# Kernel tuning notes

Hardware: AMD Instinct MI355X
Metric: run time of the kernel (lower is better)

The kernel has to match this reference:

```python
import jax, jax.numpy as jnp
import numpy as np

N = 100000
E = 3200000
NFEAT = 256
NHID = 128
NCLASS = 40
SCALE = 1.0


def setup_inputs() -> dict:
    key = jax.random.key(0)
    ks = jax.random.split(key, 8)
    x = jax.random.normal(ks[0], (N, NFEAT), dtype=jnp.float32)
    adj_row = jnp.sort(jax.random.randint(ks[1], (E,), 0, N, dtype=jnp.int32))
    adj_col = jax.random.randint(ks[2], (E,), 0, N, dtype=jnp.int32)
    adj_val = jax.random.uniform(ks[3], (E,), dtype=jnp.float32)
    # parameters (reset_parameters: weight ~ N(0,1), bias ~ N(-1,1) -> normal with mean -1? no:
    # bias.normal_(-stdv, stdv) with stdv=1 means mean=-1, std=1)
    W1 = jax.random.normal(ks[4], (NFEAT, NHID), dtype=jnp.float32)
    b1 = jax.random.normal(ks[5], (NHID,), dtype=jnp.float32) - 1.0
    W2 = jax.random.normal(ks[6], (NHID, NCLASS), dtype=jnp.float32)
    b2 = jax.random.normal(ks[7], (NCLASS,), dtype=jnp.float32) - 1.0
    return {"x": x, "adj_row": adj_row, "adj_col": adj_col, "adj_val": adj_val,
            "i": 0, "W1": W1, "b1": b1, "W2": W2, "b2": b2}


def spmm(row, col, val, dense):
    # adj @ dense where adj is sparse COO [N, N]
    gathered = val[:, None] * dense[col]          # [E, D]
    return jax.ops.segment_sum(gathered, row, num_segments=N)


def reference(x, adj_row, adj_col, adj_val, i, W1, b1, W2, b2):
    # layer 1: support = x @ W1; out = adj @ support + b1
    h = spmm(adj_row, adj_col, adj_val, x @ W1) + b1
    h = jax.nn.relu(h) * SCALE
    # dropout is identity (eval mode / training=False)
    # layer 2
    logits = spmm(adj_row, adj_col, adj_val, h @ W2) + b2
    return jax.nn.log_softmax(logits, axis=1)
```

## Files before the change

### kernel.cpp

```cpp
#include <hip/hip_runtime.h>
#include <hip/hip_bf16.h>
#include <math.h>


#define GCN_NFEAT 256
#define GCN_NHID  128
#define GCN_NCLASS 40

typedef __bf16 bf16_t;
typedef bf16_t bf16x8 __attribute__((ext_vector_type(8)));
typedef float  f32x4  __attribute__((ext_vector_type(4)));

static __device__ __forceinline__ unsigned short f2b(float f) {
    bf16_t b = (bf16_t)f;
    return *(unsigned short*)&b;
}

__global__ __launch_bounds__(256) void k_row_ptr(
    const int* __restrict__ row, int* __restrict__ row_ptr, int n_rows, int n_edges)
{
    int r = blockIdx.x * blockDim.x + threadIdx.x;
    if (r > n_rows) return;
    int lo = 0, hi = n_edges;
    while (lo < hi) {
        int mid = (lo + hi) >> 1;
        if (row[mid] < r) lo = mid + 1; else hi = mid;
    }
    row_ptr[r] = lo;
}

__global__ __launch_bounds__(256) void k_prep_w1t(
    const float* __restrict__ w1, bf16_t* __restrict__ w1t)
{
    int idx = blockIdx.x * 256 + threadIdx.x;
    int c = idx & 127;
    int k = idx >> 7;
    w1t[(size_t)c * GCN_NFEAT + k] = (bf16_t)w1[(size_t)k * GCN_NHID + c];
}

__global__ __launch_bounds__(256) void k_prep_w2t(
    const float* __restrict__ w2, bf16_t* __restrict__ w2t)
{
    int idx = blockIdx.x * 256 + threadIdx.x;
    if (idx >= 48 * GCN_NHID) return;
    int c = idx / GCN_NHID;
    int k = idx - c * GCN_NHID;
    float v = (c < GCN_NCLASS) ? w2[(size_t)k * GCN_NCLASS + c] : 0.f;
    w2t[idx] = (bf16_t)v;
}

__global__ __launch_bounds__(256) void k_gemm1(
    const float* __restrict__ x, const bf16_t* __restrict__ w1t,
    bf16_t* __restrict__ out, int nrows)
{
    __shared__ __align__(16) bf16_t As[128][72];
    __shared__ __align__(16) bf16_t Bs[128][72];

    const int tid  = threadIdx.x;
    const int wave = tid >> 6, lane = tid & 63;
    const int wm = wave >> 1, wn = wave & 1;
    const int lm = lane & 15, quad = lane >> 4;
    const int r0 = blockIdx.x * 128;

    f32x4 acc[4][4] = {};

    for (int k0 = 0; k0 < GCN_NFEAT; k0 += 64) {
        {
            const int row = tid >> 1, half = tid & 1;
            const int gr = r0 + row;
            union { bf16_t b[32]; uint4 q[4]; } t;
            if (gr < nrows) {
                const float* p = x + (size_t)gr * GCN_NFEAT + k0 + half * 32;
#pragma unroll
                for (int i = 0; i < 8; i++) {
                    float4 v = ((const float4*)p)[i];
                    t.b[i*4+0] = (bf16_t)v.x; t.b[i*4+1] = (bf16_t)v.y;
                    t.b[i*4+2] = (bf16_t)v.z; t.b[i*4+3] = (bf16_t)v.w;
                }
            } else {
#pragma unroll
                for (int i = 0; i < 4; i++) t.q[i] = make_uint4(0,0,0,0);
            }
            uint4* dst = (uint4*)&As[row][half * 32];
#pragma unroll
            for (int i = 0; i < 4; i++) dst[i] = t.q[i];
        }
        {
            const int col = tid >> 1, half = tid & 1;
            const uint4* src = (const uint4*)(w1t + (size_t)col * GCN_NFEAT + k0 + half * 32);
            uint4* dst = (uint4*)&Bs[col][half * 32];
#pragma unroll
            for (int i = 0; i < 4; i++) dst[i] = src[i];
        }
        __syncthreads();

#pragma unroll
        for (int ks = 0; ks < 2; ks++) {
            bf16x8 af[4], bfr[4];
#pragma unroll
            for (int i = 0; i < 4; i++)
                af[i] = *(const bf16x8*)&As[wm*64 + i*16 + lm][ks*32 + quad*8];
#pragma unroll
            for (int j = 0; j < 4; j++)
                bfr[j] = *(const bf16x8*)&Bs[wn*64 + j*16 + lm][ks*32 + quad*8];
#pragma unroll
            for (int i = 0; i < 4; i++)
#pragma unroll
                for (int j = 0; j < 4; j++)
                    acc[i][j] = __builtin_amdgcn_mfma_f32_16x16x32_bf16(
                        af[i], bfr[j], acc[i][j], 0, 0, 0);
        }
        __syncthreads();
    }

#pragma unroll
    for (int i = 0; i < 4; i++) {
#pragma unroll
        for (int reg = 0; reg < 4; reg++) {
            const int gr = r0 + wm*64 + i*16 + quad*4 + reg;
            if (gr < nrows) {
#pragma unroll
                for (int j = 0; j < 4; j++) {
                    const int gc = wn*64 + j*16 + lm;
                    out[(size_t)gr * GCN_NHID + gc] = (bf16_t)acc[i][j][reg];
                }
            }
        }
    }
}

__global__ __launch_bounds__(256) void k_spmm1(
    const int* __restrict__ row_ptr, const int* __restrict__ col,
    const float* __restrict__ val, const unsigned int* __restrict__ sup,
    const float* __restrict__ b1, unsigned int* __restrict__ h, int nrows)
{
    const int wid  = (blockIdx.x * blockDim.x + threadIdx.x) >> 6;
    const int lane = threadIdx.x & 63;
    if (wid >= nrows) return;
    const int e0 = row_ptr[wid];
    const int e1 = row_ptr[wid + 1];

    float ax = 0.f, ay = 0.f;
    int e = e0;
    for (; e + 3 < e1; e += 4) {
        const int c0 = col[e], c1 = col[e+1], c2 = col[e+2], c3 = col[e+3];
        const float v0 = val[e], v1 = val[e+1], v2 = val[e+2], v3 = val[e+3];
        const unsigned int u0 = sup[(size_t)c0 * 64 + lane];
        const unsigned int u1 = sup[(size_t)c1 * 64 + lane];
        const unsigned int u2 = sup[(size_t)c2 * 64 + lane];
        const unsigned int u3 = sup[(size_t)c3 * 64 + lane];
        ax = fmaf(v0, __uint_as_float(u0 << 16), ax);
        ay = fmaf(v0, __uint_as_float(u0 & 0xffff0000u), ay);
        ax = fmaf(v1, __uint_as_float(u1 << 16), ax);
        ay = fmaf(v1, __uint_as_float(u1 & 0xffff0000u), ay);
        ax = fmaf(v2, __uint_as_float(u2 << 16), ax);
        ay = fmaf(v2, __uint_as_float(u2 & 0xffff0000u), ay);
        ax = fmaf(v3, __uint_as_float(u3 << 16), ax);
        ay = fmaf(v3, __uint_as_float(u3 & 0xffff0000u), ay);
    }
    for (; e < e1; e++) {
        const unsigned int u = sup[(size_t)col[e] * 64 + lane];
        const float v = val[e];
        ax = fmaf(v, __uint_as_float(u << 16), ax);
        ay = fmaf(v, __uint_as_float(u & 0xffff0000u), ay);
    }

    const float2 bb = *(const float2*)(b1 + lane * 2);
    const float ox = fmaxf(ax + bb.x, 0.f);
    const float oy = fmaxf(ay + bb.y, 0.f);
    h[(size_t)wid * 64 + lane] = (unsigned int)f2b(ox) | ((unsigned int)f2b(oy) << 16);
}

__global__ __launch_bounds__(256) void k_gemm2(
    const bf16_t* __restrict__ h, const bf16_t* __restrict__ w2t,
    bf16_t* __restrict__ out, int nrows)
{
    __shared__ __align__(16) bf16_t As[128][136];
    __shared__ __align__(16) bf16_t Bs[48][136];

    const int tid  = threadIdx.x;
    const int wave = tid >> 6, lane = tid & 63;
    const int lm = lane & 15, quad = lane >> 4;
    const int r0 = blockIdx.x * 128;

    {
        const int row = tid >> 1, half = tid & 1;
        const int gr = r0 + row;
        uint4* dst = (uint4*)&As[row][half * 64];
        if (gr < nrows) {
            const uint4* src = (const uint4*)(h + (size_t)gr * GCN_NHID + half * 64);
#pragma unroll
            for (int i = 0; i < 8; i++) dst[i] = src[i];
        } else {
#pragma unroll
            for (int i = 0; i < 8; i++) dst[i] = make_uint4(0,0,0,0);
        }
    }
    for (int idx = tid; idx < 48 * 16; idx += 256) {
        const int c = idx >> 4, seg = idx & 15;
        ((uint4*)&Bs[c][0])[seg] = ((const uint4*)(w2t + (size_t)c * GCN_NHID))[seg];
    }
    __syncthreads();

    f32x4 acc[2][3] = {};
#pragma unroll
    for (int ks = 0; ks < 4; ks++) {
        bf16x8 af[2], bfr[3];
#pragma unroll
        for (int i = 0; i < 2; i++)
            af[i] = *(const bf16x8*)&As[wave*32 + i*16 + lm][ks*32 + quad*8];
#pragma unroll
        for (int j = 0; j < 3; j++)
            bfr[j] = *(const bf16x8*)&Bs[j*16 + lm][ks*32 + quad*8];
#pragma unroll
        for (int i = 0; i < 2; i++)
#pragma unroll
            for (int j = 0; j < 3; j++)
                acc[i][j] = __builtin_amdgcn_mfma_f32_16x16x32_bf16(
                    af[i], bfr[j], acc[i][j], 0, 0, 0);
    }

#pragma unroll
    for (int i = 0; i < 2; i++) {
#pragma unroll
        for (int reg = 0; reg < 4; reg++) {
            const int gr = r0 + wave*32 + i*16 + quad*4 + reg;
            if (gr < nrows) {
#pragma unroll
                for (int j = 0; j < 3; j++) {
                    const int gc = j*16 + lm;
                    if (gc < GCN_NCLASS)
                        out[(size_t)gr * GCN_NCLASS + gc] = (bf16_t)acc[i][j][reg];
                }
            }
        }
    }
}

__global__ __launch_bounds__(256) void k_spmm2_lsm(
    const int* __restrict__ row_ptr, const int* __restrict__ col,
    const float* __restrict__ val, const unsigned int* __restrict__ sup2,
    const float* __restrict__ b2, float* __restrict__ out, int nrows)
{
    const int wid  = (blockIdx.x * blockDim.x + threadIdx.x) >> 6;
    const int lane = threadIdx.x & 63;
    if (wid >= nrows) return;
    const int e0 = row_ptr[wid];
    const int e1 = row_ptr[wid + 1];
    const bool active = lane < (GCN_NCLASS / 2);

    float ax = 0.f, ay = 0.f;
    int e = e0;
    for (; e + 3 < e1; e += 4) {
        const int c0 = col[e], c1 = col[e+1], c2 = col[e+2], c3 = col[e+3];
        const float v0 = val[e], v1 = val[e+1], v2 = val[e+2], v3 = val[e+3];
        if (active) {
            const unsigned int u0 = sup2[(size_t)c0 * 20 + lane];
            const unsigned int u1 = sup2[(size_t)c1 * 20 + lane];
            const unsigned int u2 = sup2[(size_t)c2 * 20 + lane];
            const unsigned int u3 = sup2[(size_t)c3 * 20 + lane];
            ax = fmaf(v0, __uint_as_float(u0 << 16), ax);
            ay = fmaf(v0, __uint_as_float(u0 & 0xffff0000u), ay);
            ax = fmaf(v1, __uint_as_float(u1 << 16), ax);
            ay = fmaf(v1, __uint_as_float(u1 & 0xffff0000u), ay);
            ax = fmaf(v2, __uint_as_float(u2 << 16), ax);
            ay = fmaf(v2, __uint_as_float(u2 & 0xffff0000u), ay);
            ax = fmaf(v3, __uint_as_float(u3 << 16), ax);
            ay = fmaf(v3, __uint_as_float(u3 & 0xffff0000u), ay);
        }
    }
    for (; e < e1; e++) {
        if (active) {
            const unsigned int u = sup2[(size_t)col[e] * 20 + lane];
            const float v = val[e];
            ax = fmaf(v, __uint_as_float(u << 16), ax);
            ay = fmaf(v, __uint_as_float(u & 0xffff0000u), ay);
        }
    }

    float l0 = -INFINITY, l1 = -INFINITY;
    if (active) {
        l0 = ax + b2[lane * 2];
        l1 = ay + b2[lane * 2 + 1];
    }

    float m = fmaxf(l0, l1);
#pragma unroll
    for (int off = 32; off >= 1; off >>= 1)
        m = fmaxf(m, __shfl_xor(m, off, 64));

    float s = active ? (__expf(l0 - m) + __expf(l1 - m)) : 0.f;
#pragma unroll
    for (int off = 32; off >= 1; off >>= 1)
        s += __shfl_xor(s, off, 64);

    if (active) {
        const float lse = m + __logf(s);
        float* p = out + (size_t)wid * GCN_NCLASS + lane * 2;
        p[0] = l0 - lse;
        p[1] = l1 - lse;
    }
}

extern "C" void kernel_launch(void* const* d_in, const int* in_sizes, int n_in,
                              void* d_out, int out_size, void* d_ws, size_t ws_size,
                              hipStream_t stream)
{
    const float* x       = (const float*)d_in[0];
    const int*   adj_row = (const int*)  d_in[1];
    const int*   adj_col = (const int*)  d_in[2];
    const float* adj_val = (const float*)d_in[3];
    const float* W1 = (const float*)d_in[5];
    const float* b1 = (const float*)d_in[6];
    const float* W2 = (const float*)d_in[7];
    const float* b2 = (const float*)d_in[8];
    float* out = (float*)d_out;

    const int N = in_sizes[0] / GCN_NFEAT;
    const int E = in_sizes[1];

    char* ws = (char*)d_ws;
    size_t off = 0;
    int* row_ptr = (int*)(ws + off);
    off += (((size_t)(N + 1) * sizeof(int)) + 1023) & ~(size_t)1023;
    bf16_t* w1t = (bf16_t*)(ws + off);
    off += ((size_t)GCN_NHID * GCN_NFEAT * 2 + 1023) & ~(size_t)1023;
    bf16_t* w2t = (bf16_t*)(ws + off);
    off += ((size_t)48 * GCN_NHID * 2 + 1023) & ~(size_t)1023;
    bf16_t* sup1 = (bf16_t*)(ws + off);
    off += ((size_t)N * GCN_NHID * 2 + 1023) & ~(size_t)1023;
    bf16_t* h = (bf16_t*)(ws + off);
    bf16_t* sup2 = sup1;

    k_row_ptr<<<(N + 1 + 255) / 256, 256, 0, stream>>>(adj_row, row_ptr, N, E);
    k_prep_w1t<<<GCN_NHID * GCN_NFEAT / 256, 256, 0, stream>>>(W1, w1t);
    k_prep_w2t<<<(48 * GCN_NHID + 255) / 256, 256, 0, stream>>>(W2, w2t);
    k_gemm1<<<(N + 127) / 128, 256, 0, stream>>>(x, w1t, sup1, N);
    k_spmm1<<<(N + 3) / 4, 256, 0, stream>>>(row_ptr, adj_col, adj_val,
                                             (const unsigned int*)sup1, b1,
                                             (unsigned int*)h, N);
    k_gemm2<<<(N + 127) / 128, 256, 0, stream>>>(h, w2t, sup2, N);
    k_spmm2_lsm<<<(N + 3) / 4, 256, 0, stream>>>(row_ptr, adj_col, adj_val,
                                                 (const unsigned int*)sup2, b2, out, N);
}
```

Measured before the change: 468.6 us.

## Pack three rows per wave in spmm2 and batch-load edge indices via shuffles in spmm1

In the first SpMM, each group of 16 lanes loads 16 column indices and values at once, and the wave then broadcasts them with shuffles. This replaces the redundant scalar loads of col/val made for every edge. The second SpMM packs three output rows into one 64-lane wave, 20 lanes per row, so fewer lanes sit idle. Its log-softmax reduction becomes a segmented shuffle-down with a broadcast from each group's first lane. Rows with different edge counts in one wave now diverge, and the address math moves to 32-bit unsigned.

```diff
diff --git a/kernel.cpp b/kernel.cpp
--- a/kernel.cpp
+++ b/kernel.cpp
@@ -14,6 +14,12 @@
 static __device__ __forceinline__ unsigned short f2b(float f) {
     bf16_t b = (bf16_t)f;
     return *(unsigned short*)&b;
+}
+static __device__ __forceinline__ float blo(unsigned int u) {
+    return __uint_as_float(u << 16);
+}
+static __device__ __forceinline__ float bhi(unsigned int u) {
+    return __uint_as_float(u & 0xffff0000u);
 }
 
 __global__ __launch_bounds__(256) void k_row_ptr(
@@ -86,9 +92,9 @@
             for (int i = 0; i < 4; i++) dst[i] = t.q[i];
         }
         {
-            const int col = tid >> 1, half = tid & 1;
-            const uint4* src = (const uint4*)(w1t + (size_t)col * GCN_NFEAT + k0 + half * 32);
-            uint4* dst = (uint4*)&Bs[col][half * 32];
+            const int colc = tid >> 1, half = tid & 1;
+            const uint4* src = (const uint4*)(w1t + (size_t)colc * GCN_NFEAT + k0 + half * 32);
+            uint4* dst = (uint4*)&Bs[colc][half * 32];
 #pragma unroll
             for (int i = 0; i < 4; i++) dst[i] = src[i];
         }
@@ -139,36 +145,34 @@
     if (wid >= nrows) return;
     const int e0 = row_ptr[wid];
     const int e1 = row_ptr[wid + 1];
+    const int sub = lane & 15;
 
     float ax = 0.f, ay = 0.f;
     int e = e0;
-    for (; e + 3 < e1; e += 4) {
-        const int c0 = col[e], c1 = col[e+1], c2 = col[e+2], c3 = col[e+3];
-        const float v0 = val[e], v1 = val[e+1], v2 = val[e+2], v3 = val[e+3];
-        const unsigned int u0 = sup[(size_t)c0 * 64 + lane];
-        const unsigned int u1 = sup[(size_t)c1 * 64 + lane];
-        const unsigned int u2 = sup[(size_t)c2 * 64 + lane];
-        const unsigned int u3 = sup[(size_t)c3 * 64 + lane];
-        ax = fmaf(v0, __uint_as_float(u0 << 16), ax);
-        ay = fmaf(v0, __uint_as_float(u0 & 0xffff0000u), ay);
-        ax = fmaf(v1, __uint_as_float(u1 << 16), ax);
-        ay = fmaf(v1, __uint_as_float(u1 & 0xffff0000u), ay);
-        ax = fmaf(v2, __uint_as_float(u2 << 16), ax);
-        ay = fmaf(v2, __uint_as_float(u2 & 0xffff0000u), ay);
-        ax = fmaf(v3, __uint_as_float(u3 << 16), ax);
-        ay = fmaf(v3, __uint_as_float(u3 & 0xffff0000u), ay);
+    for (; e + 16 <= e1; e += 16) {
+        const int   cv = col[e + sub];
+        const float vv = val[e + sub];
+#pragma unroll
+        for (int j = 0; j < 16; j++) {
+            const int   cj = __shfl(cv, j, 64);
+            const float vj = __shfl(vv, j, 64);
+            const unsigned int u = sup[(unsigned)(cj << 6) + lane];
+            ax = fmaf(vj, blo(u), ax);
+            ay = fmaf(vj, bhi(u), ay);
+        }
     }
     for (; e < e1; e++) {
-        const unsigned int u = sup[(size_t)col[e] * 64 + lane];
+        const int c = col[e];
         const float v = val[e];
-        ax = fmaf(v, __uint_as_float(u << 16), ax);
-        ay = fmaf(v, __uint_as_float(u & 0xffff0000u), ay);
+        const unsigned int u = sup[(unsigned)(c << 6) + lane];
+        ax = fmaf(v, blo(u), ax);
+        ay = fmaf(v, bhi(u), ay);
     }
 
     const float2 bb = *(const float2*)(b1 + lane * 2);
     const float ox = fmaxf(ax + bb.x, 0.f);
     const float oy = fmaxf(ay + bb.y, 0.f);
-    h[(size_t)wid * 64 + lane] = (unsigned int)f2b(ox) | ((unsigned int)f2b(oy) << 16);
+    h[(unsigned)(wid << 6) + lane] = (unsigned int)f2b(ox) | ((unsigned int)f2b(oy) << 16);
 }
 
 __global__ __launch_bounds__(256) void k_gemm2(
@@ -244,59 +248,59 @@
 {
     const int wid  = (blockIdx.x * blockDim.x + threadIdx.x) >> 6;
     const int lane = threadIdx.x & 63;
-    if (wid >= nrows) return;
-    const int e0 = row_ptr[wid];
-    const int e1 = row_ptr[wid + 1];
-    const bool active = lane < (GCN_NCLASS / 2);
+    const int g    = lane / 20;
+    const int li   = lane - g * 20;
+    const int r    = wid * 3 + g;
+    const bool active = (g < 3) && (r < nrows);
+
+    int e0 = 0, e1 = 0;
+    if (active) { e0 = row_ptr[r]; e1 = row_ptr[r + 1]; }
 
     float ax = 0.f, ay = 0.f;
     int e = e0;
     for (; e + 3 < e1; e += 4) {
-        const int c0 = col[e], c1 = col[e+1], c2 = col[e+2], c3 = col[e+3];
+        const int c0 = col[e],   c1 = col[e+1], c2 = col[e+2], c3 = col[e+3];
         const float v0 = val[e], v1 = val[e+1], v2 = val[e+2], v3 = val[e+3];
-        if (active) {
-            const unsigned int u0 = sup2[(size_t)c0 * 20 + lane];
-            const unsigned int u1 = sup2[(size_t)c1 * 20 + lane];
-            const unsigned int u2 = sup2[(size_t)c2 * 20 + lane];
-            const unsigned int u3 = sup2[(size_t)c3 * 20 + lane];
-            ax = fmaf(v0, __uint_as_float(u0 << 16), ax);
-            ay = fmaf(v0, __uint_as_float(u0 & 0xffff0000u), ay);
-            ax = fmaf(v1, __uint_as_float(u1 << 16), ax);
-            ay = fmaf(v1, __uint_as_float(u1 & 0xffff0000u), ay);
-            ax = fmaf(v2, __uint_as_float(u2 << 16), ax);
-            ay = fmaf(v2, __uint_as_float(u2 & 0xffff0000u), ay);
-            ax = fmaf(v3, __uint_as_float(u3 << 16), ax);
-            ay = fmaf(v3, __uint_as_float(u3 & 0xffff0000u), ay);
-        }
+        const unsigned int u0 = sup2[(unsigned)(c0 * 20) + li];
+        const unsigned int u1 = sup2[(unsigned)(c1 * 20) + li];
+        const unsigned int u2 = sup2[(unsigned)(c2 * 20) + li];
+        const unsigned int u3 = sup2[(unsigned)(c3 * 20) + li];
+        ax = fmaf(v0, blo(u0), ax); ay = fmaf(v0, bhi(u0), ay);
+        ax = fmaf(v1, blo(u1), ax); ay = fmaf(v1, bhi(u1), ay);
+        ax = fmaf(v2, blo(u2), ax); ay = fmaf(v2, bhi(u2), ay);
+        ax = fmaf(v3, blo(u3), ax); ay = fmaf(v3, bhi(u3), ay);
     }
     for (; e < e1; e++) {
-        if (active) {
-            const unsigned int u = sup2[(size_t)col[e] * 20 + lane];
-            const float v = val[e];
-            ax = fmaf(v, __uint_as_float(u << 16), ax);
-            ay = fmaf(v, __uint_as_float(u & 0xffff0000u), ay);
-        }
+        const unsigned int u = sup2[(unsigned)(col[e] * 20) + li];
+        const float v = val[e];
+        ax = fmaf(v, blo(u), ax); ay = fmaf(v, bhi(u), ay);
     }
 
     float l0 = -INFINITY, l1 = -INFINITY;
     if (active) {
-        l0 = ax + b2[lane * 2];
-        l1 = ay + b2[lane * 2 + 1];
+        l0 = ax + b2[li * 2];
+        l1 = ay + b2[li * 2 + 1];
     }
 
     float m = fmaxf(l0, l1);
 #pragma unroll
-    for (int off = 32; off >= 1; off >>= 1)
-        m = fmaxf(m, __shfl_xor(m, off, 64));
+    for (int off = 16; off >= 1; off >>= 1) {
+        const float t = __shfl_down(m, off, 64);
+        if (li + off < 20) m = fmaxf(m, t);
+    }
+    m = __shfl(m, g * 20, 64);
 
     float s = active ? (__expf(l0 - m) + __expf(l1 - m)) : 0.f;
 #pragma unroll
-    for (int off = 32; off >= 1; off >>= 1)
-        s += __shfl_xor(s, off, 64);
+    for (int off = 16; off >= 1; off >>= 1) {
+        const float t = __shfl_down(s, off, 64);
+        if (li + off < 20) s += t;
+    }
+    s = __shfl(s, g * 20, 64);
 
     if (active) {
         const float lse = m + __logf(s);
-        float* p = out + (size_t)wid * GCN_NCLASS + lane * 2;
+        float* p = out + (size_t)r * GCN_NCLASS + li * 2;
         p[0] = l0 - lse;
         p[1] = l1 - lse;
     }
@@ -340,6 +344,7 @@
                                              (const unsigned int*)sup1, b1,
                                              (unsigned int*)h, N);
     k_gemm2<<<(N + 127) / 128, 256, 0, stream>>>(h, w2t, sup2, N);
-    k_spmm2_lsm<<<(N + 3) / 4, 256, 0, stream>>>(row_ptr, adj_col, adj_val,
-                                                 (const unsigned int*)sup2, b2, out, N);
-}
+    const int nw2 = (N + 2) / 3;
+    k_spmm2_lsm<<<(nw2 + 3) / 4, 256, 0, stream>>>(row_ptr, adj_col, adj_val,
+                                                   (const unsigned int*)sup2, b2, out, N);
+}
```

Measured after the change: 417.3 us. -10.9%, faster.
